# Performance work log

Measured on AMD Instinct MI355X. Metric: run time of the kernel, lower is better.

Reference implementation:

```python
import jax, jax.numpy as jnp
import numpy as np

N_NODES = 100000
N_EDGES = 1000000
HID = 128


def _lin(x, W, b):
    # torch nn.Linear: x @ W.T + b
    return x @ W.T + b


def _comp_agg(n_feat, e_vec, s, d, n_nodes):
    """u_sub_e message + sum aggregation + in-degree^-0.5 normalization."""
    msg = n_feat[s] - e_vec[None, :]                     # [E, D]
    agg = jax.ops.segment_sum(msg, d, num_segments=n_nodes)  # [N, D]
    deg = jax.ops.segment_sum(jnp.ones_like(d, dtype=n_feat.dtype), d,
                              num_segments=n_nodes)      # in-degrees
    norm = jnp.maximum(deg, 1.0) ** -0.5
    return agg * norm[:, None]


def setup_inputs() -> dict:
    key = jax.random.key(0)
    ks = jax.random.split(key, 16)
    sc = 1.0 / np.sqrt(HID)
    return {
        "n_feat": jax.random.normal(ks[0], (N_NODES, HID), jnp.float32),
        "e_feat_fwd": jax.random.normal(ks[1], (HID,), jnp.float32),
        "e_feat_rev": jax.random.normal(ks[2], (HID,), jnp.float32),
        "W_I": jax.random.normal(ks[3], (HID, HID), jnp.float32) * sc,
        "b_I": jax.random.normal(ks[4], (HID,), jnp.float32) * sc,
        "W_O": jax.random.normal(ks[5], (HID, HID), jnp.float32) * sc,
        "b_O": jax.random.normal(ks[6], (HID,), jnp.float32) * sc,
        "W_S": jax.random.normal(ks[7], (HID, HID), jnp.float32) * sc,
        "b_S": jax.random.normal(ks[8], (HID,), jnp.float32) * sc,
        "W_rel": jax.random.normal(ks[9], (HID, HID), jnp.float32) * sc,
        "b_rel": jax.random.normal(ks[10], (HID,), jnp.float32) * sc,
        "src": jax.random.randint(ks[11], (N_EDGES,), 0, N_NODES, jnp.int32),
        "dst": jax.random.randint(ks[12], (N_EDGES,), 0, N_NODES, jnp.int32),
    }


def reference(n_feat, e_feat_fwd, e_feat_rev, W_I, b_I, W_O, b_O,
              W_S, b_S, W_rel, b_rel, src, dst):
    n_nodes = n_feat.shape[0]
    # forward relation: edges src->dst, composed with e_feat_fwd, then W_I
    comp_f = _comp_agg(n_feat, e_feat_fwd, src, dst, n_nodes)
    h_f = _lin(comp_f, W_I, b_I)
    # reverse relation ('_inv'): edges dst->src, composed with e_feat_rev, then W_O
    comp_r = _comp_agg(n_feat, e_feat_rev, dst, src, n_nodes)
    h_r = _lin(comp_r, W_O, b_O)
    # self-loop path
    h_s = _lin(n_feat, W_S, b_S)
    # mix: dropout is identity at p=0.0; activation is None
    n_out = (h_f + h_r) * (2.0 / 3.0) + h_s * (1.0 / 3.0)
    # edge feature update (formula 2)
    e_out_fwd = _lin(e_feat_fwd, W_rel, b_rel)
    e_out_rev = _lin(e_feat_rev, W_rel, b_rel)
    return (n_out, e_out_fwd, e_out_rev)
```

## Files before the change

### kernel.cpp

```cpp
#include <hip/hip_runtime.h>
#include <stdint.h>

#define NN 100000
#define NE 1000000
#define HID 128
#define NB 391

typedef __attribute__((ext_vector_type(4))) float f32x4;
typedef __attribute__((ext_vector_type(4))) unsigned u32x4;
typedef __attribute__((ext_vector_type(8))) short short8;
typedef __attribute__((ext_vector_type(8))) __bf16 bf16x8;

union V8 { short8 s; bf16x8 b; };
union AW { unsigned w[4]; bf16x8 b; };
union BP { struct { unsigned long long lo, hi; } u; short8 s; bf16x8 b; };

__device__ __forceinline__ unsigned short f2bf(float f) {
    unsigned u = __float_as_uint(f);
    unsigned r = u + 0x7fffu + ((u >> 16) & 1u);
    return (unsigned short)(r >> 16);
}

__global__ __launch_bounds__(256) void k_prep(
        const float* __restrict__ n_feat, unsigned* __restrict__ nfbf_u,
        const float* __restrict__ WI, const float* __restrict__ WO,
        const float* __restrict__ WS, const float* __restrict__ bI,
        const float* __restrict__ bO, const float* __restrict__ bS,
        unsigned short* __restrict__ Wbf, float* __restrict__ biasc,
        const float* __restrict__ W_rel, const float* __restrict__ b_rel,
        const float* __restrict__ e_fwd, const float* __restrict__ e_rev,
        const int* __restrict__ src, const int* __restrict__ dst,
        int* __restrict__ bcntD, int* __restrict__ bcntS,
        float* __restrict__ outp) {
    __shared__ int hD[NB], hS[NB];
    int bb = blockIdx.x;
    int tid = threadIdx.x;
    const int NC = NN * HID / 8 / 256;

    if (bb < NC) {
        int t = bb * 256 + tid;
        const f32x4* pin = (const f32x4*)n_feat;
        f32x4 a = pin[2 * t], b = pin[2 * t + 1];
        u32x4 o;
        o[0] = (unsigned)f2bf(a[0]) | ((unsigned)f2bf(a[1]) << 16);
        o[1] = (unsigned)f2bf(a[2]) | ((unsigned)f2bf(a[3]) << 16);
        o[2] = (unsigned)f2bf(b[0]) | ((unsigned)f2bf(b[1]) << 16);
        o[3] = (unsigned)f2bf(b[2]) | ((unsigned)f2bf(b[3]) << 16);
        ((u32x4*)nfbf_u)[t] = o;
    } else if (bb < NC + 192) {
        int t = (bb - NC) * 256 + tid;
        int p = t >> 14, i = t & 16383;
        const float* Wsrc = (p == 0) ? WI : ((p == 1) ? WO : WS);
        float scale = (p == 2) ? (1.0f / 3.0f) : (2.0f / 3.0f);
        Wbf[t] = f2bf(Wsrc[i] * scale);
        if (t < HID) biasc[t] = (2.0f / 3.0f) * (bI[t] + bO[t]) + (1.0f / 3.0f) * bS[t];
    } else if (bb == NC + 192) {
        int cc = tid & 127;
        const float* e = (tid < 128) ? e_fwd : e_rev;
        float s = b_rel[cc];
        #pragma unroll 4
        for (int k = 0; k < HID; ++k) s += W_rel[cc * HID + k] * e[k];
        outp[(size_t)NN * HID + ((tid < 128) ? 0 : HID) + cc] = s;
    } else if (bb == NC + 193) {
        if (tid < 64) nfbf_u[(size_t)NN * 64 + tid] = 0;
    } else {
        for (int b = tid; b < NB; b += 256) { hD[b] = 0; hS[b] = 0; }
        __syncthreads();
        int base = (bb - NC - 194) * 8192;
        #pragma unroll
        for (int i = 0; i < 32; ++i) {
            int e = base + i * 256 + tid;
            if (e < NE) {
                atomicAdd(&hD[dst[e] >> 8], 1);
                atomicAdd(&hS[src[e] >> 8], 1);
            }
        }
        __syncthreads();
        for (int b = tid; b < NB; b += 256) {
            if (hD[b]) atomicAdd(&bcntD[b], hD[b]);
            if (hS[b]) atomicAdd(&bcntS[b], hS[b]);
        }
    }
}

__global__ __launch_bounds__(512) void k_bucketscan(
        const int* __restrict__ bcntD, const int* __restrict__ bcntS,
        int* __restrict__ bbaseD, int* __restrict__ bbaseS,
        int* __restrict__ bcurD, int* __restrict__ bcurS) {
    __shared__ int wtot[8];
    int t = threadIdx.x, lane = t & 63, w = t >> 6;
    #pragma unroll
    for (int dir = 0; dir < 2; ++dir) {
        const int* cnt = dir ? bcntS : bcntD;
        int* bb = dir ? bbaseS : bbaseD;
        int* bc = dir ? bcurS : bcurD;
        int v = (t < NB) ? cnt[t] : 0;
        int x = v;
        #pragma unroll
        for (int off = 1; off < 64; off <<= 1) {
            int y = __shfl_up(x, off);
            if (lane >= off) x += y;
        }
        if (lane == 63) wtot[w] = x;
        __syncthreads();
        int wbase = 0;
        for (int j = 0; j < w; ++j) wbase += wtot[j];
        int incl = wbase + x;
        if (t < NB) { bb[t] = incl - v; bc[t] = incl - v; }
        if (t == NB - 1) bb[NB] = incl;
        __syncthreads();
    }
}

__global__ __launch_bounds__(256) void k_binfill(
        const int* __restrict__ src, const int* __restrict__ dst,
        int* __restrict__ bcurD, int* __restrict__ bcurS,
        unsigned* __restrict__ binD, unsigned* __restrict__ binS) {
    __shared__ int hD[NB], hS[NB];
    int tid = threadIdx.x;
    for (int b = tid; b < NB; b += 256) { hD[b] = 0; hS[b] = 0; }
    __syncthreads();
    int base = blockIdx.x * 8192;
    int s[32], d[32];
    #pragma unroll
    for (int i = 0; i < 32; ++i) {
        int e = base + i * 256 + tid;
        s[i] = -1; d[i] = -1;
        if (e < NE) { s[i] = src[e]; d[i] = dst[e]; }
    }
    #pragma unroll
    for (int i = 0; i < 32; ++i) {
        if (s[i] >= 0) {
            atomicAdd(&hD[d[i] >> 8], 1);
            atomicAdd(&hS[s[i] >> 8], 1);
        }
    }
    __syncthreads();
    for (int b = tid; b < NB; b += 256) {
        int c = hD[b];
        hD[b] = c ? atomicAdd(&bcurD[b], c) : 0;
        c = hS[b];
        hS[b] = c ? atomicAdd(&bcurS[b], c) : 0;
    }
    __syncthreads();
    #pragma unroll
    for (int i = 0; i < 32; ++i) {
        if (s[i] >= 0) {
            int p = atomicAdd(&hD[d[i] >> 8], 1);
            binD[p] = ((unsigned)s[i] << 8) | ((unsigned)d[i] & 255u);
            int q = atomicAdd(&hS[s[i] >> 8], 1);
            binS[q] = ((unsigned)d[i] << 8) | ((unsigned)s[i] & 255u);
        }
    }
}

__global__ __launch_bounds__(256) void k_bucketsort(
        const unsigned* __restrict__ binD, const unsigned* __restrict__ binS,
        const int* __restrict__ bbaseD, const int* __restrict__ bbaseS,
        int* __restrict__ row_in, int* __restrict__ row_out,
        int* __restrict__ col_in, int* __restrict__ col_out,
        unsigned char* __restrict__ dloc_in, unsigned char* __restrict__ dloc_out) {
    __shared__ int c[256];
    __shared__ int wtot[4];
    int bid = blockIdx.x;
    int dir = (bid >= NB) ? 1 : 0;
    int b = dir ? (bid - NB) : bid;
    const unsigned* bin = dir ? binS : binD;
    const int* bb = dir ? bbaseS : bbaseD;
    int* row = dir ? row_out : row_in;
    int* col = dir ? col_out : col_in;
    unsigned char* dlc = dir ? dloc_out : dloc_in;

    int tid = threadIdx.x, lane = tid & 63, w = tid >> 6;
    int base = bb[b], cnt = bb[b + 1] - base;
    int node0 = b << 8;
    int M = NN - node0; if (M > 256) M = 256;

    c[tid] = 0;
    __syncthreads();
    for (int k = tid; k < cnt; k += 256)
        atomicAdd(&c[bin[base + k] & 255u], 1);
    __syncthreads();
    int v = c[tid];
    int x = v;
    #pragma unroll
    for (int off = 1; off < 64; off <<= 1) {
        int y = __shfl_up(x, off);
        if (lane >= off) x += y;
    }
    if (lane == 63) wtot[w] = x;
    __syncthreads();
    int wbase = 0;
    for (int j = 0; j < w; ++j) wbase += wtot[j];
    int incl = wbase + x;
    if (tid < M) row[node0 + tid + 1] = base + incl;
    if (b == 0 && tid == 0) row[0] = 0;
    __syncthreads();
    c[tid] = base + incl - v;
    __syncthreads();
    for (int k = tid; k < cnt; k += 256) {
        unsigned pk = bin[base + k];
        int p = atomicAdd(&c[pk & 255u], 1);
        col[p] = (int)(pk >> 8);
        dlc[p] = (unsigned char)(pk & 15u);
    }
}

typedef __attribute__((address_space(3))) unsigned char as3u8;
typedef __attribute__((address_space(3))) unsigned as3u32;
typedef __attribute__((address_space(1))) const unsigned as1cu32;

__global__ __launch_bounds__(256) void k_agg(
        const unsigned char* __restrict__ nf,
        const float* __restrict__ e_fwd, const float* __restrict__ e_rev,
        const int* __restrict__ row_in, const int* __restrict__ col_in,
        const unsigned char* __restrict__ dloc_in,
        const int* __restrict__ row_out, const int* __restrict__ col_out,
        const unsigned char* __restrict__ dloc_out,
        const unsigned short* __restrict__ Wbf, const float* __restrict__ biasc,
        float* __restrict__ outp) {
    __shared__ __align__(1024) unsigned char smem[4][8192];
    int warp = threadIdx.x >> 6;
    int l = threadIdx.x & 63;
    int gbase = blockIdx.x * 2;
    int dir = warp & 1;
    int grp = gbase + (warp >> 1);
    int node0 = grp << 4;

    const int* row = dir ? row_out : row_in;
    const int* col = dir ? col_out : col_in;
    const unsigned char* dloc = dir ? dloc_out : dloc_in;
    const float* ev = dir ? e_rev : e_fwd;

    int h = l & 1;
    int kslot = l >> 1;
    int lm = l & 15;
    int q = l >> 4;
    int kg = q * 8;

    as3u8* ldsp = (as3u8*)&smem[warp][0];
    as3u8* trp  = ldsp + ((lm << 3) + (q << 8));

    int ebase = row[node0];
    int eend  = row[node0 + 16];

    f32x4 acc[8];
    #pragma unroll
    for (int nb = 0; nb < 8; ++nb) {
        acc[nb][0] = 0.0f; acc[nb][1] = 0.0f; acc[nb][2] = 0.0f; acc[nb][3] = 0.0f;
    }

    while (ebase < eend) {
        int e = ebase + (l & 31);
        int rowid = (e < eend) ? col[e] : NN;
        int dl    = (e < eend) ? (int)dloc[e] : 255;
        int rowk  = __shfl(rowid, kslot);
        const unsigned char* gp = nf + (((size_t)rowk) << 8) + (h << 4);
#define GLL(I) __builtin_amdgcn_global_load_lds( \
            (as1cu32*)(gp + (I) * 32), \
            (as3u32*)(ldsp + (I) * 1024), 16, 0, 0)
        GLL(0); GLL(1); GLL(2); GLL(3); GLL(4); GLL(5); GLL(6); GLL(7);
#undef GLL

        AW a;
        #pragma unroll
        for (int j2 = 0; j2 < 4; ++j2) {
            int d0 = __shfl(dl, kg + 2 * j2);
            int d1 = __shfl(dl, kg + 2 * j2 + 1);
            unsigned lo = (d0 == lm) ? 0x3F80u : 0u;
            unsigned hi = (d1 == lm) ? 0x3F80u : 0u;
            a.w[j2] = lo | (hi << 16);
        }

        asm volatile("s_waitcnt vmcnt(0)" ::: "memory");
        __builtin_amdgcn_sched_barrier(0);

        unsigned long long t0[8], t1[8];
        #pragma unroll
        for (int nb = 0; nb < 8; ++nb) {
            asm volatile("ds_read_b64_tr_b16 %0, %1 offset:%2"
                         : "=&v"(t0[nb]) : "v"(trp), "i"(nb * 1024));
            asm volatile("ds_read_b64_tr_b16 %0, %1 offset:%2"
                         : "=&v"(t1[nb]) : "v"(trp), "i"(nb * 1024 + 128));
        }
        asm volatile("s_waitcnt lgkmcnt(0)" ::: "memory");
        __builtin_amdgcn_sched_barrier(0);

        #pragma unroll
        for (int nb = 0; nb < 8; ++nb) {
            BP bp;
            bp.u.lo = t0[nb];
            bp.u.hi = t1[nb];
            acc[nb] = __builtin_amdgcn_mfma_f32_16x16x32_bf16(a.b, bp.b, acc[nb], 0, 0, 0);
        }
        ebase += 32;
    }

    int rp = row[node0 + ((l < 17) ? l : 16)];
    int degi = __shfl(rp, l + 1) - rp;
    float degfv = (float)degi;
    float rnv = (degi > 0) ? (1.0f / sqrtf(degfv)) : 1.0f;

    float evv[8];
    #pragma unroll
    for (int nb = 0; nb < 8; ++nb) evv[nb] = ev[nb * 16 + lm];

    #pragma unroll
    for (int ip = 0; ip < 2; ++ip) {
        int m0 = q * 4 + 2 * ip;
        float dm0 = __shfl(degfv, m0), rm0 = __shfl(rnv, m0);
        float dm1 = __shfl(degfv, m0 + 1), rm1 = __shfl(rnv, m0 + 1);
        #pragma unroll
        for (int nb = 0; nb < 8; ++nb) {
            float v0 = (acc[nb][2 * ip]     - dm0 * evv[nb]) * rm0;
            float v1 = (acc[nb][2 * ip + 1] - dm1 * evv[nb]) * rm1;
            unsigned dw = (unsigned)f2bf(v0) | ((unsigned)f2bf(v1) << 16);
            *(as3u32*)(ldsp + (nb * 16 + lm) * 32 + q * 8 + ip * 4) = dw;
        }
    }
    __syncthreads();

    const unsigned short* nfu = (const unsigned short*)nf;
    int obase = warp * 2;
    f32x4 D[2][2];
    #pragma unroll
    for (int a2 = 0; a2 < 2; ++a2)
        #pragma unroll
        for (int b2 = 0; b2 < 2; ++b2) {
            D[a2][b2][0] = 0.0f; D[a2][b2][1] = 0.0f;
            D[a2][b2][2] = 0.0f; D[a2][b2][3] = 0.0f;
        }

    #pragma unroll
    for (int p = 0; p < 3; ++p) {
        V8 A[2][4];
        #pragma unroll
        for (int ob2 = 0; ob2 < 2; ++ob2)
            #pragma unroll
            for (int kb = 0; kb < 4; ++kb)
                A[ob2][kb].s = *(const short8*)(Wbf + p * 16384 +
                    ((obase + ob2) * 16 + lm) * 128 + kb * 32 + q * 8);
        #pragma unroll
        for (int gg = 0; gg < 2; ++gg) {
            BP B[4];
            if (p < 2) {
                unsigned long long tb0[4], tb1[4];
                as3u8* ib = (as3u8*)&smem[gg * 2 + p][0] + ((lm << 3) + (q << 8));
                #pragma unroll
                for (int kb = 0; kb < 4; ++kb) {
                    asm volatile("ds_read_b64_tr_b16 %0, %1 offset:%2"
                                 : "=&v"(tb0[kb]) : "v"(ib), "i"(kb * 1024));
                    asm volatile("ds_read_b64_tr_b16 %0, %1 offset:%2"
                                 : "=&v"(tb1[kb]) : "v"(ib), "i"(kb * 1024 + 128));
                }
                asm volatile("s_waitcnt lgkmcnt(0)" ::: "memory");
                __builtin_amdgcn_sched_barrier(0);
                #pragma unroll
                for (int kb = 0; kb < 4; ++kb) { B[kb].u.lo = tb0[kb]; B[kb].u.hi = tb1[kb]; }
            } else {
                int node = (gbase + gg) * 16 + lm;
                #pragma unroll
                for (int kb = 0; kb < 4; ++kb)
                    B[kb].s = *(const short8*)(nfu + (size_t)node * 128 + kb * 32 + q * 8);
            }
            #pragma unroll
            for (int ob2 = 0; ob2 < 2; ++ob2)
                #pragma unroll
                for (int kb = 0; kb < 4; ++kb)
                    D[ob2][gg] = __builtin_amdgcn_mfma_f32_16x16x32_bf16(
                        A[ob2][kb].b, B[kb].b, D[ob2][gg], 0, 0, 0);
        }
    }

    #pragma unroll
    for (int ob2 = 0; ob2 < 2; ++ob2) {
        int o0 = (obase + ob2) * 16 + q * 4;
        f32x4 bias = *(const f32x4*)(biasc + o0);
        #pragma unroll
        for (int gg = 0; gg < 2; ++gg) {
            int node = (gbase + gg) * 16 + lm;
            f32x4 r = D[ob2][gg] + bias;
            *(f32x4*)(outp + (size_t)node * 128 + o0) = r;
        }
    }
}

extern "C" void kernel_launch(void* const* d_in, const int* in_sizes, int n_in,
                              void* d_out, int out_size, void* d_ws, size_t ws_size,
                              hipStream_t stream) {
    const float* n_feat = (const float*)d_in[0];
    const float* e_fwd  = (const float*)d_in[1];
    const float* e_rev  = (const float*)d_in[2];
    const float* W_I    = (const float*)d_in[3];
    const float* b_I    = (const float*)d_in[4];
    const float* W_O    = (const float*)d_in[5];
    const float* b_O    = (const float*)d_in[6];
    const float* W_S    = (const float*)d_in[7];
    const float* b_S    = (const float*)d_in[8];
    const float* W_rel  = (const float*)d_in[9];
    const float* b_rel  = (const float*)d_in[10];
    const int*   src    = (const int*)d_in[11];
    const int*   dst    = (const int*)d_in[12];
    float* outp = (float*)d_out;

    uint8_t* ws = (uint8_t*)d_ws;
    size_t off = 0;
    auto alloc = [&](size_t bytes) -> size_t {
        size_t r = off;
        off = (off + bytes + 255) & ~(size_t)255;
        return r;
    };
    size_t o_nfbf   = alloc((size_t)(NN + 1) * HID * 2);
    size_t o_wbf    = alloc((size_t)3 * HID * HID * 2);
    size_t o_biasc  = alloc(HID * 4);
    size_t o_rowin  = alloc((size_t)(NN + 1) * 4);
    size_t o_rowout = alloc((size_t)(NN + 1) * 4);
    size_t o_colin  = alloc((size_t)NE * 4);
    size_t o_colout = alloc((size_t)NE * 4);
    size_t o_dlin   = alloc((size_t)NE);
    size_t o_dlout  = alloc((size_t)NE);
    size_t o_binD   = alloc((size_t)NE * 4);
    size_t o_binS   = alloc((size_t)NE * 4);
    size_t o_bcnt   = alloc((size_t)2 * NB * 4);
    size_t o_bbaseD = alloc((size_t)(NB + 1) * 4);
    size_t o_bbaseS = alloc((size_t)(NB + 1) * 4);
    size_t o_bcurD  = alloc((size_t)NB * 4);
    size_t o_bcurS  = alloc((size_t)NB * 4);
    (void)ws_size; (void)in_sizes; (void)n_in; (void)out_size;

    unsigned short* nfbf  = (unsigned short*)(ws + o_nfbf);
    unsigned short* wbf   = (unsigned short*)(ws + o_wbf);
    float*     biasc      = (float*)(ws + o_biasc);
    int* row_in  = (int*)(ws + o_rowin);
    int* row_out = (int*)(ws + o_rowout);
    int* col_in  = (int*)(ws + o_colin);
    int* col_out = (int*)(ws + o_colout);
    unsigned char* dloc_in  = (unsigned char*)(ws + o_dlin);
    unsigned char* dloc_out = (unsigned char*)(ws + o_dlout);
    unsigned* binD = (unsigned*)(ws + o_binD);
    unsigned* binS = (unsigned*)(ws + o_binS);
    int* bcntD   = (int*)(ws + o_bcnt);
    int* bcntS   = bcntD + NB;
    int* bbaseD  = (int*)(ws + o_bbaseD);
    int* bbaseS  = (int*)(ws + o_bbaseS);
    int* bcurD   = (int*)(ws + o_bcurD);
    int* bcurS   = (int*)(ws + o_bcurS);

    (void)hipMemsetAsync(ws + o_bcnt, 0, (size_t)2 * NB * 4, stream);

    k_prep<<<6567, 256, 0, stream>>>(n_feat, (unsigned*)nfbf,
                                     W_I, W_O, W_S, b_I, b_O, b_S, wbf, biasc,
                                     W_rel, b_rel, e_fwd, e_rev,
                                     src, dst, bcntD, bcntS, outp);

    k_bucketscan<<<1, 512, 0, stream>>>(bcntD, bcntS, bbaseD, bbaseS, bcurD, bcurS);
    k_binfill<<<(NE + 8191) / 8192, 256, 0, stream>>>(src, dst, bcurD, bcurS, binD, binS);
    k_bucketsort<<<2 * NB, 256, 0, stream>>>(binD, binS, bbaseD, bbaseS,
                                             row_in, row_out, col_in, col_out,
                                             dloc_in, dloc_out);

    k_agg<<<3125, 256, 0, stream>>>((const unsigned char*)nfbf, e_fwd, e_rev,
                                    row_in, col_in, dloc_in,
                                    row_out, col_out, dloc_out,
                                    wbf, biasc, outp);
}
```

Baseline: 193.4 us.

## Pack column and local-dest into one word, 16-edge steps with prefetch

Merges the separate column index and local destination byte arrays into one packed 32-bit word, so each edge needs a single load. The aggregation loop now handles 16 edges per step instead of 32, with two lanes per row each loading 64-byte halves. The next step's packed indices are prefetched while the current gather is in flight, and per-warp LDS staging is halved. Half of the MFMA K dimension is now zero-filled, so tensor-core work per edge doubles and there are twice as many loop iterations.

```diff
diff --git a/kernel.cpp b/kernel.cpp
--- a/kernel.cpp
+++ b/kernel.cpp
@@ -158,8 +158,7 @@
         const unsigned* __restrict__ binD, const unsigned* __restrict__ binS,
         const int* __restrict__ bbaseD, const int* __restrict__ bbaseS,
         int* __restrict__ row_in, int* __restrict__ row_out,
-        int* __restrict__ col_in, int* __restrict__ col_out,
-        unsigned char* __restrict__ dloc_in, unsigned char* __restrict__ dloc_out) {
+        unsigned* __restrict__ col2_in, unsigned* __restrict__ col2_out) {
     __shared__ int c[256];
     __shared__ int wtot[4];
     int bid = blockIdx.x;
@@ -168,8 +167,7 @@
     const unsigned* bin = dir ? binS : binD;
     const int* bb = dir ? bbaseS : bbaseD;
     int* row = dir ? row_out : row_in;
-    int* col = dir ? col_out : col_in;
-    unsigned char* dlc = dir ? dloc_out : dloc_in;
+    unsigned* col2 = dir ? col2_out : col2_in;
 
     int tid = threadIdx.x, lane = tid & 63, w = tid >> 6;
     int base = bb[b], cnt = bb[b + 1] - base;
@@ -201,8 +199,7 @@
     for (int k = tid; k < cnt; k += 256) {
         unsigned pk = bin[base + k];
         int p = atomicAdd(&c[pk & 255u], 1);
-        col[p] = (int)(pk >> 8);
-        dlc[p] = (unsigned char)(pk & 15u);
+        col2[p] = ((pk >> 8) << 4) | (pk & 15u);
     }
 }
 
@@ -213,13 +210,11 @@
 __global__ __launch_bounds__(256) void k_agg(
         const unsigned char* __restrict__ nf,
         const float* __restrict__ e_fwd, const float* __restrict__ e_rev,
-        const int* __restrict__ row_in, const int* __restrict__ col_in,
-        const unsigned char* __restrict__ dloc_in,
-        const int* __restrict__ row_out, const int* __restrict__ col_out,
-        const unsigned char* __restrict__ dloc_out,
+        const int* __restrict__ row_in, const unsigned* __restrict__ col2_in,
+        const int* __restrict__ row_out, const unsigned* __restrict__ col2_out,
         const unsigned short* __restrict__ Wbf, const float* __restrict__ biasc,
         float* __restrict__ outp) {
-    __shared__ __align__(1024) unsigned char smem[4][8192];
+    __shared__ __align__(1024) unsigned char smem[4][4096];
     int warp = threadIdx.x >> 6;
     int l = threadIdx.x & 63;
     int gbase = blockIdx.x * 2;
@@ -228,21 +223,20 @@
     int node0 = grp << 4;
 
     const int* row = dir ? row_out : row_in;
-    const int* col = dir ? col_out : col_in;
-    const unsigned char* dloc = dir ? dloc_out : dloc_in;
+    const unsigned* col2 = dir ? col2_out : col2_in;
     const float* ev = dir ? e_rev : e_fwd;
 
-    int h = l & 1;
-    int kslot = l >> 1;
     int lm = l & 15;
     int q = l >> 4;
     int kg = q * 8;
+    int la = l & 15;
+    int kslot = (l & 31) >> 1;
 
     as3u8* ldsp = (as3u8*)&smem[warp][0];
-    as3u8* trp  = ldsp + ((lm << 3) + (q << 8));
-
-    int ebase = row[node0];
-    int eend  = row[node0 + 16];
+    as3u8* trp  = ldsp + (((q & 1) << 8) + (lm << 3));
+
+    int ecur = row[node0];
+    int eend = row[node0 + 16];
 
     f32x4 acc[8];
     #pragma unroll
@@ -250,25 +244,29 @@
         acc[nb][0] = 0.0f; acc[nb][1] = 0.0f; acc[nb][2] = 0.0f; acc[nb][3] = 0.0f;
     }
 
-    while (ebase < eend) {
-        int e = ebase + (l & 31);
-        int rowid = (e < eend) ? col[e] : NN;
-        int dl    = (e < eend) ? (int)dloc[e] : 255;
-        int rowk  = __shfl(rowid, kslot);
-        const unsigned char* gp = nf + (((size_t)rowk) << 8) + (h << 4);
+    unsigned pk = (ecur + la < eend) ? col2[ecur + la] : ((unsigned)NN << 4);
+    while (ecur < eend) {
+        int enext = ecur + 16;
+        int rowk = __shfl((int)(pk >> 4), kslot);
+        const unsigned char* gp = nf + (((size_t)rowk) << 8) +
+                                  ((l >> 5) << 5) + ((l & 1) << 4);
 #define GLL(I) __builtin_amdgcn_global_load_lds( \
-            (as1cu32*)(gp + (I) * 32), \
+            (as1cu32*)(gp + (I) * 64), \
             (as3u32*)(ldsp + (I) * 1024), 16, 0, 0)
-        GLL(0); GLL(1); GLL(2); GLL(3); GLL(4); GLL(5); GLL(6); GLL(7);
+        GLL(0); GLL(1); GLL(2); GLL(3);
 #undef GLL
-
+        unsigned pknext = (enext < eend)
+            ? ((enext + la < eend) ? col2[enext + la] : ((unsigned)NN << 4))
+            : 0u;
+
+        int dl = (int)(pk & 15u);
         AW a;
         #pragma unroll
         for (int j2 = 0; j2 < 4; ++j2) {
             int d0 = __shfl(dl, kg + 2 * j2);
             int d1 = __shfl(dl, kg + 2 * j2 + 1);
-            unsigned lo = (d0 == lm) ? 0x3F80u : 0u;
-            unsigned hi = (d1 == lm) ? 0x3F80u : 0u;
+            unsigned lo = (q < 2 && d0 == lm) ? 0x3F80u : 0u;
+            unsigned hi = (q < 2 && d1 == lm) ? 0x3F80u : 0u;
             a.w[j2] = lo | (hi << 16);
         }
 
@@ -279,9 +277,9 @@
         #pragma unroll
         for (int nb = 0; nb < 8; ++nb) {
             asm volatile("ds_read_b64_tr_b16 %0, %1 offset:%2"
-                         : "=&v"(t0[nb]) : "v"(trp), "i"(nb * 1024));
+                         : "=&v"(t0[nb]) : "v"(trp), "i"(nb * 512));
             asm volatile("ds_read_b64_tr_b16 %0, %1 offset:%2"
-                         : "=&v"(t1[nb]) : "v"(trp), "i"(nb * 1024 + 128));
+                         : "=&v"(t1[nb]) : "v"(trp), "i"(nb * 512 + 128));
         }
         asm volatile("s_waitcnt lgkmcnt(0)" ::: "memory");
         __builtin_amdgcn_sched_barrier(0);
@@ -293,7 +291,8 @@
             bp.u.hi = t1[nb];
             acc[nb] = __builtin_amdgcn_mfma_f32_16x16x32_bf16(a.b, bp.b, acc[nb], 0, 0, 0);
         }
-        ebase += 32;
+        pk = pknext;
+        ecur = enext;
     }
 
     int rp = row[node0 + ((l < 17) ? l : 16)];
@@ -415,10 +414,8 @@
     size_t o_biasc  = alloc(HID * 4);
     size_t o_rowin  = alloc((size_t)(NN + 1) * 4);
     size_t o_rowout = alloc((size_t)(NN + 1) * 4);
-    size_t o_colin  = alloc((size_t)NE * 4);
-    size_t o_colout = alloc((size_t)NE * 4);
-    size_t o_dlin   = alloc((size_t)NE);
-    size_t o_dlout  = alloc((size_t)NE);
+    size_t o_col2in = alloc((size_t)NE * 4);
+    size_t o_col2out= alloc((size_t)NE * 4);
     size_t o_binD   = alloc((size_t)NE * 4);
     size_t o_binS   = alloc((size_t)NE * 4);
     size_t o_bcnt   = alloc((size_t)2 * NB * 4);
@@ -433,10 +430,8 @@
     float*     biasc      = (float*)(ws + o_biasc);
     int* row_in  = (int*)(ws + o_rowin);
     int* row_out = (int*)(ws + o_rowout);
-    int* col_in  = (int*)(ws + o_colin);
-    int* col_out = (int*)(ws + o_colout);
-    unsigned char* dloc_in  = (unsigned char*)(ws + o_dlin);
-    unsigned char* dloc_out = (unsigned char*)(ws + o_dlout);
+    unsigned* col2_in  = (unsigned*)(ws + o_col2in);
+    unsigned* col2_out = (unsigned*)(ws + o_col2out);
     unsigned* binD = (unsigned*)(ws + o_binD);
     unsigned* binS = (unsigned*)(ws + o_binS);
     int* bcntD   = (int*)(ws + o_bcnt);
@@ -456,11 +451,9 @@
     k_bucketscan<<<1, 512, 0, stream>>>(bcntD, bcntS, bbaseD, bbaseS, bcurD, bcurS);
     k_binfill<<<(NE + 8191) / 8192, 256, 0, stream>>>(src, dst, bcurD, bcurS, binD, binS);
     k_bucketsort<<<2 * NB, 256, 0, stream>>>(binD, binS, bbaseD, bbaseS,
-                                             row_in, row_out, col_in, col_out,
-                                             dloc_in, dloc_out);
+                                             row_in, row_out, col2_in, col2_out);
 
     k_agg<<<3125, 256, 0, stream>>>((const unsigned char*)nfbf, e_fwd, e_rev,
-                                    row_in, col_in, dloc_in,
-                                    row_out, col_out, dloc_out,
+                                    row_in, col2_in, row_out, col2_out,
                                     wbf, biasc, outp);
 }
```

Result: faster. 189.4 us (-2.0%).
